# Optimization experiments

Hardware: AMD Instinct MI355X
Metric: run time of the kernel (lower is better)

The kernel has to match this reference:

```python
import jax, jax.numpy as jnp
import numpy as np
import math

B, S, HID = 2, 2048, 2048
NH, NKV = 32, 8
HD = HID // NH  # 64
N_REP = NH // NKV  # 4


def setup_inputs() -> dict:
    key = jax.random.key(0)
    ks = jax.random.split(key, 7)
    sc = 0.02
    return {
        "hidden_states": jax.random.normal(ks[0], (B, S, HID), jnp.float32),
        "cos": jax.random.normal(ks[1], (S, HD), jnp.float32),
        "sin": jax.random.normal(ks[2], (S, HD), jnp.float32),
        "wq": jax.random.normal(ks[3], (NH * HD, HID), jnp.float32) * sc,
        "wk": jax.random.normal(ks[4], (NKV * HD, HID), jnp.float32) * sc,
        "wv": jax.random.normal(ks[5], (NKV * HD, HID), jnp.float32) * sc,
        "wo": jax.random.normal(ks[6], (HID, NH * HD), jnp.float32) * sc,
    }


def _rotate_half(x):
    x1, x2 = jnp.split(x, 2, axis=-1)
    return jnp.concatenate([-x2, x1], axis=-1)


def _apply_rotary(q, k, cos, sin):
    # q: [B,S,NH,HD], k: [B,S,NKV,HD]; cos/sin: [S,HD] broadcast over batch, heads
    c = cos[None, :, None, :]
    s = sin[None, :, None, :]
    return q * c + _rotate_half(q) * s, k * c + _rotate_half(k) * s


def reference(hidden_states, cos, sin, wq, wk, wv, wo):
    x = hidden_states  # [B,S,HID]
    q = jnp.einsum('bsh,dh->bsd', x, wq).reshape(B, S, NH, HD)
    k = jnp.einsum('bsh,dh->bsd', x, wk).reshape(B, S, NKV, HD)
    v = jnp.einsum('bsh,dh->bsd', x, wv).reshape(B, S, NKV, HD)
    q, k = _apply_rotary(q, k, cos, sin)
    # repeat_kv: expand kv heads by N_REP -> [B,S,NH,HD]
    k = jnp.repeat(k, N_REP, axis=2)
    v = jnp.repeat(v, N_REP, axis=2)
    # [B,NH,S,HD]
    q = q.transpose(0, 2, 1, 3)
    k = k.transpose(0, 2, 1, 3)
    v = v.transpose(0, 2, 1, 3)
    scores = jnp.einsum('bhqd,bhkd->bhqk', q, k) / math.sqrt(HD)
    probs = jax.nn.softmax(scores.astype(jnp.float32), axis=-1).astype(q.dtype)
    out = jnp.einsum('bhqk,bhkd->bhqd', probs, v)
    out = out.transpose(0, 2, 1, 3).reshape(B, S, NH * HD)
    return jnp.einsum('bsd,hd->bsh', out, wo)
```

## Files before the change

kernel.cpp:

```cpp
#include <hip/hip_runtime.h>
#include <math.h>

#define B 2
#define S 2048
#define HID 2048
#define NH 32
#define NKV 8
#define HD 64
#define NREP 4

typedef __bf16 bf16_t;
typedef bf16_t bf16x8 __attribute__((ext_vector_type(8)));
typedef float floatx4 __attribute__((ext_vector_type(4)));

__device__ __forceinline__ void gld_lds16(const void* g, void* l) {
    __builtin_amdgcn_global_load_lds(
        (const __attribute__((address_space(1))) void*)g,
        (__attribute__((address_space(3))) void*)l, 16, 0, 0);
}

__global__ __launch_bounds__(256) void cast_f32_bf16(const float* __restrict__ src,
                                                     bf16_t* __restrict__ dst, int n) {
    int i = (blockIdx.x * 256 + threadIdx.x) * 8;
    if (i >= n) return;
    float4 f0 = *(const float4*)(src + i);
    float4 f1 = *(const float4*)(src + i + 4);
    bf16x8 v;
    v[0] = (bf16_t)f0.x; v[1] = (bf16_t)f0.y; v[2] = (bf16_t)f0.z; v[3] = (bf16_t)f0.w;
    v[4] = (bf16_t)f1.x; v[5] = (bf16_t)f1.y; v[6] = (bf16_t)f1.z; v[7] = (bf16_t)f1.w;
    *(bf16x8*)(dst + i) = v;
}

#define TM 128
#define TN 128
#define BK 32

enum { MODE_QKV = 0, MODE_OUT = 2 };

template <int MODE>
__global__ __launch_bounds__(256) void gemm_mfma(const bf16_t* __restrict__ A,
                                                 const bf16_t* __restrict__ W,
                                                 void* __restrict__ outQ,
                                                 bf16_t* __restrict__ outK,
                                                 bf16_t* __restrict__ outV,
                                                 const float* __restrict__ cosp,
                                                 const float* __restrict__ sinp,
                                                 int M, int N, int K) {
    __shared__ __align__(16) bf16_t As[TM * BK];
    __shared__ __align__(16) bf16_t Ws[TN * BK];
    const int t    = threadIdx.x;
    const int wave = t >> 6, lane = t & 63;
    const int quad = lane >> 4, l16 = lane & 15;
    const int m0 = blockIdx.y * TM, n0 = blockIdx.x * TN;
    const int wm = (wave >> 1) * 64, wn = (wave & 1) * 64;

    floatx4 zero4 = {0.f, 0.f, 0.f, 0.f};
    floatx4 acc[4][4];
    #pragma unroll
    for (int i = 0; i < 4; ++i)
        #pragma unroll
        for (int j = 0; j < 4; ++j) acc[i][j] = zero4;

    const bf16_t* Arow = A + (size_t)(m0 + (t >> 2)) * K + (t & 3) * 8;
    const bf16_t* Wrow = W + (size_t)(n0 + (t >> 2)) * K + (t & 3) * 8;
    bf16_t* Asl = As + t * 8;
    bf16_t* Wsl = Ws + t * 8;

    for (int k0 = 0; k0 < K; k0 += BK) {
        gld_lds16(Arow + k0,          Asl);
        gld_lds16(Arow + 64 * K + k0, Asl + 64 * BK);
        gld_lds16(Wrow + k0,          Wsl);
        gld_lds16(Wrow + 64 * K + k0, Wsl + 64 * BK);
        __syncthreads();
        bf16x8 af[4], bfr[4];
        #pragma unroll
        for (int i = 0; i < 4; ++i)
            af[i] = *(bf16x8*)&As[(wm + i * 16 + l16) * BK + quad * 8];
        #pragma unroll
        for (int j = 0; j < 4; ++j)
            bfr[j] = *(bf16x8*)&Ws[(wn + j * 16 + l16) * BK + quad * 8];
        #pragma unroll
        for (int i = 0; i < 4; ++i)
            #pragma unroll
            for (int j = 0; j < 4; ++j)
                acc[i][j] = __builtin_amdgcn_mfma_f32_16x16x32_bf16(af[i], bfr[j], acc[i][j], 0, 0, 0);
        __syncthreads();
    }

    if constexpr (MODE == MODE_OUT) {
        float* C = (float*)outQ;
        #pragma unroll
        for (int i = 0; i < 4; ++i)
            #pragma unroll
            for (int r = 0; r < 4; ++r) {
                int row = m0 + wm + i * 16 + quad * 4 + r;
                #pragma unroll
                for (int j = 0; j < 4; ++j)
                    C[(size_t)row * N + n0 + wn + j * 16 + l16] = acc[i][j][r];
            }
    } else {
        const int hh = (n0 + wn) / 64;
        #pragma unroll
        for (int i = 0; i < 4; ++i)
            #pragma unroll
            for (int r = 0; r < 4; ++r) {
                int m = m0 + wm + i * 16 + quad * 4 + r;
                int b = m / S, s = m % S;
                if (hh < NH + NKV) {
                    bf16_t* base;
                    float sc;
                    if (hh < NH) {
                        base = (bf16_t*)outQ + ((size_t)(b * NH + hh) * S + s) * HD;
                        sc = 0.125f;
                    } else {
                        base = outK + ((size_t)(b * NKV + (hh - NH)) * S + s) * HD;
                        sc = 1.0f;
                    }
                    #pragma unroll
                    for (int j = 0; j < 2; ++j) {
                        int d = j * 16 + l16;
                        float x1 = acc[i][j][r], x2 = acc[i][j + 2][r];
                        float c1 = cosp[s * HD + d],      s1 = sinp[s * HD + d];
                        float c2 = cosp[s * HD + d + 32], s2 = sinp[s * HD + d + 32];
                        base[d]      = (bf16_t)((x1 * c1 - x2 * s1) * sc);
                        base[d + 32] = (bf16_t)((x2 * c2 + x1 * s2) * sc);
                    }
                } else {
                    int kvh = hh - NH - NKV;
                    bf16_t* vb = outV + ((size_t)(b * NKV + kvh) * HD) * S + s;
                    #pragma unroll
                    for (int j = 0; j < 4; ++j)
                        vb[(size_t)(j * 16 + l16) * S] = (bf16_t)acc[i][j][r];
                }
            }
    }
}

#define PP 72
__global__ __launch_bounds__(256, 2) void attn_mfma(const bf16_t* __restrict__ Q,
                                                    const bf16_t* __restrict__ Kb,
                                                    const bf16_t* __restrict__ Vt,
                                                    bf16_t* __restrict__ Ob) {
    __shared__ __align__(16) bf16_t Ks[2 * 64 * 32];
    __shared__ __align__(16) bf16_t Vs[2 * 64 * 32];
    __shared__ __align__(16) bf16_t Ps[4 * 64 * PP];
    const int t    = threadIdx.x;
    const int wave = t >> 6, lane = t & 63;
    const int quad = lane >> 4, l16 = lane & 15;
    const int bh = blockIdx.y, b = bh / NH, h = bh % NH, kvh = h / NREP;
    const int q0 = blockIdx.x * 256;

    const bf16_t* qbase = Q + ((size_t)bh * S + q0 + wave * 64) * HD;
    const bf16_t* kbase = Kb + ((size_t)(b * NKV + kvh) * S) * HD;
    const bf16_t* vbase = Vt + (size_t)(b * NKV + kvh) * HD * S;
    bf16_t* Psw = Ps + wave * 64 * PP;

    bf16x8 qf[4][2];
    #pragma unroll
    for (int i = 0; i < 4; ++i)
        #pragma unroll
        for (int ks = 0; ks < 2; ++ks)
            qf[i][ks] = *(const bf16x8*)(qbase + (size_t)(i * 16 + l16) * HD + ks * 32 + quad * 8);

    floatx4 zero4 = {0.f, 0.f, 0.f, 0.f};
    floatx4 of[4][4];
    #pragma unroll
    for (int i = 0; i < 4; ++i)
        #pragma unroll
        for (int n = 0; n < 4; ++n) of[i][n] = zero4;
    float lsum[4][4];
    #pragma unroll
    for (int i = 0; i < 4; ++i)
        #pragma unroll
        for (int r = 0; r < 4; ++r) lsum[i][r] = 0.f;

    const int r4 = t >> 2;
    const int c8 = (t & 3) * 8;

    for (int kt = 0; kt < S; kt += 64) {
        __syncthreads();
        gld_lds16(kbase + (size_t)(kt + r4) * HD + c8,      Ks + t * 8);
        gld_lds16(kbase + (size_t)(kt + r4) * HD + 32 + c8, Ks + 2048 + t * 8);
        gld_lds16(vbase + (size_t)r4 * S + kt + c8,         Vs + t * 8);
        gld_lds16(vbase + (size_t)r4 * S + kt + 32 + c8,    Vs + 2048 + t * 8);
        __syncthreads();

        bf16x8 bk[2][4];
        #pragma unroll
        for (int ks = 0; ks < 2; ++ks)
            #pragma unroll
            for (int j = 0; j < 4; ++j)
                bk[ks][j] = *(bf16x8*)&Ks[ks * 2048 + (j * 16 + l16) * 32 + quad * 8];

        #pragma unroll
        for (int i = 0; i < 4; ++i) {
            floatx4 sf[4];
            #pragma unroll
            for (int j = 0; j < 4; ++j) sf[j] = zero4;
            #pragma unroll
            for (int ks = 0; ks < 2; ++ks)
                #pragma unroll
                for (int j = 0; j < 4; ++j)
                    sf[j] = __builtin_amdgcn_mfma_f32_16x16x32_bf16(qf[i][ks], bk[ks][j], sf[j], 0, 0, 0);
            #pragma unroll
            for (int r = 0; r < 4; ++r) {
                float p0 = __expf(sf[0][r]), p1 = __expf(sf[1][r]);
                float p2 = __expf(sf[2][r]), p3 = __expf(sf[3][r]);
                lsum[i][r] += (p0 + p1) + (p2 + p3);
                int row = i * 16 + quad * 4 + r;
                Psw[row * PP + 0  + l16] = (bf16_t)p0;
                Psw[row * PP + 16 + l16] = (bf16_t)p1;
                Psw[row * PP + 32 + l16] = (bf16_t)p2;
                Psw[row * PP + 48 + l16] = (bf16_t)p3;
            }
        }

        #pragma unroll
        for (int ks = 0; ks < 2; ++ks) {
            bf16x8 vb[4], pa[4];
            #pragma unroll
            for (int n = 0; n < 4; ++n)
                vb[n] = *(bf16x8*)&Vs[ks * 2048 + (n * 16 + l16) * 32 + quad * 8];
            #pragma unroll
            for (int i = 0; i < 4; ++i)
                pa[i] = *(bf16x8*)&Psw[(i * 16 + l16) * PP + ks * 32 + quad * 8];
            #pragma unroll
            for (int i = 0; i < 4; ++i)
                #pragma unroll
                for (int n = 0; n < 4; ++n)
                    of[i][n] = __builtin_amdgcn_mfma_f32_16x16x32_bf16(pa[i], vb[n], of[i][n], 0, 0, 0);
        }
    }

    #pragma unroll
    for (int i = 0; i < 4; ++i)
        #pragma unroll
        for (int r = 0; r < 4; ++r) {
            float ls = lsum[i][r];
            #pragma unroll
            for (int off = 1; off < 16; off <<= 1) ls += __shfl_xor(ls, off);
            float inv = 1.f / ls;
            int q = q0 + wave * 64 + i * 16 + quad * 4 + r;
            bf16_t* ob = Ob + ((size_t)(b * S + q)) * HID + h * HD;
            #pragma unroll
            for (int n = 0; n < 4; ++n) ob[n * 16 + l16] = (bf16_t)(of[i][n][r] * inv);
        }
}

extern "C" void kernel_launch(void* const* d_in, const int* in_sizes, int n_in,
                              void* d_out, int out_size, void* d_ws, size_t ws_size,
                              hipStream_t stream) {
    const float* x    = (const float*)d_in[0];
    const float* cosp = (const float*)d_in[1];
    const float* sinp = (const float*)d_in[2];
    const float* wq   = (const float*)d_in[3];
    const float* wk   = (const float*)d_in[4];
    const float* wv   = (const float*)d_in[5];
    const float* wo   = (const float*)d_in[6];
    float* out = (float*)d_out;

    char* ws = (char*)d_ws;
    bf16_t* xb    = (bf16_t*)(ws);
    bf16_t* kb    = (bf16_t*)(ws + 16777216);
    bf16_t* vtb   = (bf16_t*)(ws + 20971520);
    bf16_t* wqkvb = (bf16_t*)(ws + 25165824);
    bf16_t* attb  = (bf16_t*)(ws);
    bf16_t* wob   = (bf16_t*)(ws + 25165824);
    bf16_t* qb    = (bf16_t*)d_out;

    const int M = B * S;

    cast_f32_bf16<<<4096, 256, 0, stream>>>(x, xb, B * S * HID);
    cast_f32_bf16<<<2048, 256, 0, stream>>>(wq, wqkvb, NH * HD * HID);
    cast_f32_bf16<<<512,  256, 0, stream>>>(wk, wqkvb + (size_t)2048 * HID, NKV * HD * HID);
    cast_f32_bf16<<<512,  256, 0, stream>>>(wv, wqkvb + (size_t)2560 * HID, NKV * HD * HID);

    gemm_mfma<MODE_QKV><<<dim3(3072 / TN, M / TM), 256, 0, stream>>>(
        xb, wqkvb, (void*)qb, kb, vtb, cosp, sinp, M, 3072, HID);

    cast_f32_bf16<<<2048, 256, 0, stream>>>(wo, wob, HID * NH * HD);

    attn_mfma<<<dim3(S / 256, B * NH), 256, 0, stream>>>(qb, kb, vtb, attb);

    gemm_mfma<MODE_OUT><<<dim3(2048 / TN, M / TM), 256, 0, stream>>>(
        attb, wob, (void*)out, nullptr, nullptr, nullptr, nullptr, M, 2048, HID);
}
```

Before: 358.2 us.

## Transpose attention MFMA operands, use exp2 softmax, merge casts, shrink attention blocks

Attention now computes S^T = K·Q^T and O^T = V^T·P^T. That lets each lane write its P values as packed 4-element bf16 stores and the output as packed int2 stores. It also cuts the row-sum reduction to two shuffles. The softmax uses exp2, with log2(e) folded into the Q scale in the QKV epilogue. Attention blocks shrink to 128 threads (2 waves), giving twice as many blocks but half the K/V tile reuse per block. All five f32-to-bf16 casts are merged into one launch, and wo gets its own workspace region so its cast can run early.

Result: faster. 333.5 us (-6.9%).

```diff
diff --git a/kernel.cpp b/kernel.cpp
--- a/kernel.cpp
+++ b/kernel.cpp
@@ -11,6 +11,7 @@
 
 typedef __bf16 bf16_t;
 typedef bf16_t bf16x8 __attribute__((ext_vector_type(8)));
+typedef bf16_t bf16x2 __attribute__((ext_vector_type(2)));
 typedef float floatx4 __attribute__((ext_vector_type(4)));
 
 __device__ __forceinline__ void gld_lds16(const void* g, void* l) {
@@ -19,10 +20,27 @@
         (__attribute__((address_space(3))) void*)l, 16, 0, 0);
 }
 
-__global__ __launch_bounds__(256) void cast_f32_bf16(const float* __restrict__ src,
-                                                     bf16_t* __restrict__ dst, int n) {
-    int i = (blockIdx.x * 256 + threadIdx.x) * 8;
-    if (i >= n) return;
+__device__ __forceinline__ int pack2(float a, float b) {
+    bf16x2 v; v[0] = (bf16_t)a; v[1] = (bf16_t)b;
+    return __builtin_bit_cast(int, v);
+}
+
+__global__ __launch_bounds__(256) void cast_all(const float* __restrict__ x,
+                                                const float* __restrict__ wq,
+                                                const float* __restrict__ wk,
+                                                const float* __restrict__ wv,
+                                                const float* __restrict__ wo,
+                                                bf16_t* __restrict__ xb,
+                                                bf16_t* __restrict__ wqkvb,
+                                                bf16_t* __restrict__ wob) {
+    int gid = blockIdx.x * 256 + threadIdx.x;
+    const float* src; bf16_t* dst; int idx;
+    if (gid < 1048576)      { src = x;  dst = xb;               idx = gid; }
+    else if (gid < 1572864) { src = wq; dst = wqkvb;            idx = gid - 1048576; }
+    else if (gid < 1703936) { src = wk; dst = wqkvb + 4194304;  idx = gid - 1572864; }
+    else if (gid < 1835008) { src = wv; dst = wqkvb + 5242880;  idx = gid - 1703936; }
+    else                    { src = wo; dst = wob;              idx = gid - 1835008; }
+    size_t i = (size_t)idx * 8;
     float4 f0 = *(const float4*)(src + i);
     float4 f1 = *(const float4*)(src + i + 4);
     bf16x8 v;
@@ -111,7 +129,7 @@
                     float sc;
                     if (hh < NH) {
                         base = (bf16_t*)outQ + ((size_t)(b * NH + hh) * S + s) * HD;
-                        sc = 0.125f;
+                        sc = 0.18033688011f;
                     } else {
                         base = outK + ((size_t)(b * NKV + (hh - NH)) * S + s) * HD;
                         sc = 1.0f;
@@ -137,114 +155,111 @@
 }
 
 #define PP 72
-__global__ __launch_bounds__(256, 2) void attn_mfma(const bf16_t* __restrict__ Q,
+__global__ __launch_bounds__(128, 2) void attn_mfma(const bf16_t* __restrict__ Q,
                                                     const bf16_t* __restrict__ Kb,
                                                     const bf16_t* __restrict__ Vt,
                                                     bf16_t* __restrict__ Ob) {
     __shared__ __align__(16) bf16_t Ks[2 * 64 * 32];
     __shared__ __align__(16) bf16_t Vs[2 * 64 * 32];
-    __shared__ __align__(16) bf16_t Ps[4 * 64 * PP];
+    __shared__ __align__(16) bf16_t Pq[2 * 64 * PP];
     const int t    = threadIdx.x;
     const int wave = t >> 6, lane = t & 63;
     const int quad = lane >> 4, l16 = lane & 15;
     const int bh = blockIdx.y, b = bh / NH, h = bh % NH, kvh = h / NREP;
-    const int q0 = blockIdx.x * 256;
+    const int q0 = blockIdx.x * 128;
 
     const bf16_t* qbase = Q + ((size_t)bh * S + q0 + wave * 64) * HD;
     const bf16_t* kbase = Kb + ((size_t)(b * NKV + kvh) * S) * HD;
     const bf16_t* vbase = Vt + (size_t)(b * NKV + kvh) * HD * S;
-    bf16_t* Psw = Ps + wave * 64 * PP;
+    bf16_t* Pqw = Pq + wave * 64 * PP;
 
     bf16x8 qf[4][2];
     #pragma unroll
-    for (int i = 0; i < 4; ++i)
+    for (int qj = 0; qj < 4; ++qj)
         #pragma unroll
         for (int ks = 0; ks < 2; ++ks)
-            qf[i][ks] = *(const bf16x8*)(qbase + (size_t)(i * 16 + l16) * HD + ks * 32 + quad * 8);
+            qf[qj][ks] = *(const bf16x8*)(qbase + (size_t)(qj * 16 + l16) * HD + ks * 32 + quad * 8);
 
     floatx4 zero4 = {0.f, 0.f, 0.f, 0.f};
     floatx4 of[4][4];
     #pragma unroll
-    for (int i = 0; i < 4; ++i)
-        #pragma unroll
-        for (int n = 0; n < 4; ++n) of[i][n] = zero4;
-    float lsum[4][4];
-    #pragma unroll
-    for (int i = 0; i < 4; ++i)
-        #pragma unroll
-        for (int r = 0; r < 4; ++r) lsum[i][r] = 0.f;
+    for (int di = 0; di < 4; ++di)
+        #pragma unroll
+        for (int qj = 0; qj < 4; ++qj) of[di][qj] = zero4;
+    float lsum[4] = {0.f, 0.f, 0.f, 0.f};
 
     const int r4 = t >> 2;
     const int c8 = (t & 3) * 8;
 
     for (int kt = 0; kt < S; kt += 64) {
         __syncthreads();
-        gld_lds16(kbase + (size_t)(kt + r4) * HD + c8,      Ks + t * 8);
-        gld_lds16(kbase + (size_t)(kt + r4) * HD + 32 + c8, Ks + 2048 + t * 8);
-        gld_lds16(vbase + (size_t)r4 * S + kt + c8,         Vs + t * 8);
-        gld_lds16(vbase + (size_t)r4 * S + kt + 32 + c8,    Vs + 2048 + t * 8);
-        __syncthreads();
-
-        bf16x8 bk[2][4];
-        #pragma unroll
-        for (int ks = 0; ks < 2; ++ks)
-            #pragma unroll
-            for (int j = 0; j < 4; ++j)
-                bk[ks][j] = *(bf16x8*)&Ks[ks * 2048 + (j * 16 + l16) * 32 + quad * 8];
-
-        #pragma unroll
-        for (int i = 0; i < 4; ++i) {
+        #pragma unroll
+        for (int ks = 0; ks < 2; ++ks) {
+            gld_lds16(kbase + (size_t)(kt + r4) * HD + ks * 32 + c8,      Ks + ks * 2048 + t * 8);
+            gld_lds16(kbase + (size_t)(kt + 32 + r4) * HD + ks * 32 + c8, Ks + ks * 2048 + 1024 + t * 8);
+            gld_lds16(vbase + (size_t)r4 * S + kt + ks * 32 + c8,         Vs + ks * 2048 + t * 8);
+            gld_lds16(vbase + (size_t)(32 + r4) * S + kt + ks * 32 + c8,  Vs + ks * 2048 + 1024 + t * 8);
+        }
+        __syncthreads();
+
+        #pragma unroll
+        for (int ki = 0; ki < 4; ++ki) {
+            bf16x8 ka0 = *(bf16x8*)&Ks[0 * 2048 + (ki * 16 + l16) * 32 + quad * 8];
+            bf16x8 ka1 = *(bf16x8*)&Ks[1 * 2048 + (ki * 16 + l16) * 32 + quad * 8];
             floatx4 sf[4];
             #pragma unroll
-            for (int j = 0; j < 4; ++j) sf[j] = zero4;
-            #pragma unroll
-            for (int ks = 0; ks < 2; ++ks)
+            for (int qj = 0; qj < 4; ++qj) sf[qj] = zero4;
+            #pragma unroll
+            for (int qj = 0; qj < 4; ++qj)
+                sf[qj] = __builtin_amdgcn_mfma_f32_16x16x32_bf16(ka0, qf[qj][0], sf[qj], 0, 0, 0);
+            #pragma unroll
+            for (int qj = 0; qj < 4; ++qj)
+                sf[qj] = __builtin_amdgcn_mfma_f32_16x16x32_bf16(ka1, qf[qj][1], sf[qj], 0, 0, 0);
+            #pragma unroll
+            for (int qj = 0; qj < 4; ++qj) {
+                float p0 = __builtin_amdgcn_exp2f(sf[qj][0]);
+                float p1 = __builtin_amdgcn_exp2f(sf[qj][1]);
+                float p2 = __builtin_amdgcn_exp2f(sf[qj][2]);
+                float p3 = __builtin_amdgcn_exp2f(sf[qj][3]);
+                lsum[qj] += (p0 + p1) + (p2 + p3);
+                int2 pk; pk.x = pack2(p0, p1); pk.y = pack2(p2, p3);
+                *(int2*)&Pqw[(qj * 16 + l16) * PP + ki * 16 + quad * 4] = pk;
+            }
+        }
+
+        #pragma unroll
+        for (int ks = 0; ks < 2; ++ks) {
+            bf16x8 pb[4], va[4];
+            #pragma unroll
+            for (int qj = 0; qj < 4; ++qj)
+                pb[qj] = *(bf16x8*)&Pqw[(qj * 16 + l16) * PP + ks * 32 + quad * 8];
+            #pragma unroll
+            for (int di = 0; di < 4; ++di)
+                va[di] = *(bf16x8*)&Vs[ks * 2048 + (di * 16 + l16) * 32 + quad * 8];
+            #pragma unroll
+            for (int di = 0; di < 4; ++di)
                 #pragma unroll
-                for (int j = 0; j < 4; ++j)
-                    sf[j] = __builtin_amdgcn_mfma_f32_16x16x32_bf16(qf[i][ks], bk[ks][j], sf[j], 0, 0, 0);
-            #pragma unroll
-            for (int r = 0; r < 4; ++r) {
-                float p0 = __expf(sf[0][r]), p1 = __expf(sf[1][r]);
-                float p2 = __expf(sf[2][r]), p3 = __expf(sf[3][r]);
-                lsum[i][r] += (p0 + p1) + (p2 + p3);
-                int row = i * 16 + quad * 4 + r;
-                Psw[row * PP + 0  + l16] = (bf16_t)p0;
-                Psw[row * PP + 16 + l16] = (bf16_t)p1;
-                Psw[row * PP + 32 + l16] = (bf16_t)p2;
-                Psw[row * PP + 48 + l16] = (bf16_t)p3;
-            }
-        }
-
-        #pragma unroll
-        for (int ks = 0; ks < 2; ++ks) {
-            bf16x8 vb[4], pa[4];
-            #pragma unroll
-            for (int n = 0; n < 4; ++n)
-                vb[n] = *(bf16x8*)&Vs[ks * 2048 + (n * 16 + l16) * 32 + quad * 8];
-            #pragma unroll
-            for (int i = 0; i < 4; ++i)
-                pa[i] = *(bf16x8*)&Psw[(i * 16 + l16) * PP + ks * 32 + quad * 8];
-            #pragma unroll
-            for (int i = 0; i < 4; ++i)
-                #pragma unroll
-                for (int n = 0; n < 4; ++n)
-                    of[i][n] = __builtin_amdgcn_mfma_f32_16x16x32_bf16(pa[i], vb[n], of[i][n], 0, 0, 0);
-        }
-    }
-
-    #pragma unroll
-    for (int i = 0; i < 4; ++i)
-        #pragma unroll
-        for (int r = 0; r < 4; ++r) {
-            float ls = lsum[i][r];
-            #pragma unroll
-            for (int off = 1; off < 16; off <<= 1) ls += __shfl_xor(ls, off);
-            float inv = 1.f / ls;
-            int q = q0 + wave * 64 + i * 16 + quad * 4 + r;
-            bf16_t* ob = Ob + ((size_t)(b * S + q)) * HID + h * HD;
-            #pragma unroll
-            for (int n = 0; n < 4; ++n) ob[n * 16 + l16] = (bf16_t)(of[i][n][r] * inv);
-        }
+                for (int qj = 0; qj < 4; ++qj)
+                    of[di][qj] = __builtin_amdgcn_mfma_f32_16x16x32_bf16(va[di], pb[qj], of[di][qj], 0, 0, 0);
+        }
+    }
+
+    #pragma unroll
+    for (int qj = 0; qj < 4; ++qj) {
+        float ls = lsum[qj];
+        ls += __shfl_xor(ls, 16);
+        ls += __shfl_xor(ls, 32);
+        float inv = 1.f / ls;
+        int q = q0 + wave * 64 + qj * 16 + l16;
+        bf16_t* ob = Ob + ((size_t)(b * S + q)) * HID + h * HD;
+        #pragma unroll
+        for (int di = 0; di < 4; ++di) {
+            int2 pk;
+            pk.x = pack2(of[di][qj][0] * inv, of[di][qj][1] * inv);
+            pk.y = pack2(of[di][qj][2] * inv, of[di][qj][3] * inv);
+            *(int2*)(ob + di * 16 + quad * 4) = pk;
+        }
+    }
 }
 
 extern "C" void kernel_launch(void* const* d_in, const int* in_sizes, int n_in,
@@ -264,23 +279,18 @@
     bf16_t* kb    = (bf16_t*)(ws + 16777216);
     bf16_t* vtb   = (bf16_t*)(ws + 20971520);
     bf16_t* wqkvb = (bf16_t*)(ws + 25165824);
+    bf16_t* wob   = (bf16_t*)(ws + 37748736);
     bf16_t* attb  = (bf16_t*)(ws);
-    bf16_t* wob   = (bf16_t*)(ws + 25165824);
     bf16_t* qb    = (bf16_t*)d_out;
 
     const int M = B * S;
 
-    cast_f32_bf16<<<4096, 256, 0, stream>>>(x, xb, B * S * HID);
-    cast_f32_bf16<<<2048, 256, 0, stream>>>(wq, wqkvb, NH * HD * HID);
-    cast_f32_bf16<<<512,  256, 0, stream>>>(wk, wqkvb + (size_t)2048 * HID, NKV * HD * HID);
-    cast_f32_bf16<<<512,  256, 0, stream>>>(wv, wqkvb + (size_t)2560 * HID, NKV * HD * HID);
+    cast_all<<<9216, 256, 0, stream>>>(x, wq, wk, wv, wo, xb, wqkvb, wob);
 
     gemm_mfma<MODE_QKV><<<dim3(3072 / TN, M / TM), 256, 0, stream>>>(
         xb, wqkvb, (void*)qb, kb, vtb, cosp, sinp, M, 3072, HID);
 
-    cast_f32_bf16<<<2048, 256, 0, stream>>>(wo, wob, HID * NH * HD);
-
-    attn_mfma<<<dim3(S / 256, B * NH), 256, 0, stream>>>(qb, kb, vtb, attb);
+    attn_mfma<<<dim3(S / 128, B * NH), 128, 0, stream>>>(qb, kb, vtb, attb);
 
     gemm_mfma<MODE_OUT><<<dim3(2048 / TN, M / TM), 256, 0, stream>>>(
         attb, wob, (void*)out, nullptr, nullptr, nullptr, nullptr, M, 2048, HID);
```
